# Optimization experiments

Measured on AMD Instinct MI355X. Metric: run time of the kernel, lower is better.

## Reference

```python
import jax, jax.numpy as jnp
import numpy as np
from jax import lax

DN = ('NHWC', 'HWIO', 'NHWC')
OUTPUT_STRIDE = 2
PEAK_THRESHOLD = 0.2


def setup_inputs() -> dict:
    key = jax.random.key(0)
    k1, k2, k3 = jax.random.split(key, 3)
    crops = jax.random.normal(k1, (128, 192, 192, 1), dtype=jnp.float32)
    # simple confmap backbone: stride-2 conv -> relu -> 3x3 conv to 17 nodes
    W1 = jax.random.normal(k2, (3, 3, 1, 32), dtype=jnp.float32) * 0.1
    b1 = jnp.zeros((32,), dtype=jnp.float32)
    W2 = jax.random.normal(k3, (3, 3, 32, 17), dtype=jnp.float32) * 0.1
    b2 = jnp.zeros((17,), dtype=jnp.float32)
    return {"crops": crops, "W1": W1, "b1": b1, "W2": W2, "b2": b2}


def _confmaps(crops, W1, b1, W2, b2):
    # keras_model forward: (B, 192, 192, 1) -> (B, 96, 96, 17), output_stride = 2
    h = lax.conv_general_dilated(crops, W1, (2, 2), 'SAME', dimension_numbers=DN) + b1
    h = jax.nn.relu(h)
    cms = lax.conv_general_dilated(h, W2, (1, 1), 'SAME', dimension_numbers=DN) + b2
    return cms


def _find_global_peaks_local(cms, threshold):
    # cms: (B, H, W, N) -> peaks (B, N, 2) in (x, y), vals (B, N)
    B, H, W, N = cms.shape
    cm = jnp.transpose(cms, (0, 3, 1, 2)).reshape(B, N, H * W)  # (B, N, HW)
    flat_idx = jnp.argmax(cm, axis=-1)                           # (B, N)
    vals = jnp.take_along_axis(cm, flat_idx[..., None], axis=-1)[..., 0]
    yi = flat_idx // W
    xi = flat_idx % W

    def gather(yy, xx):
        yy = jnp.clip(yy, 0, H - 1)
        xx = jnp.clip(xx, 0, W - 1)
        return jnp.take_along_axis(cm, (yy * W + xx)[..., None], axis=-1)[..., 0]

    # quarter-pixel local gradient offset (refinement='local')
    dx = 0.25 * jnp.sign(gather(yi, xi + 1) - gather(yi, xi - 1))
    dy = 0.25 * jnp.sign(gather(yi + 1, xi) - gather(yi - 1, xi))

    pts = jnp.stack([xi.astype(cm.dtype) + dx, yi.astype(cm.dtype) + dy], axis=-1)
    pts = jnp.where(vals[..., None] >= threshold, pts, jnp.nan)
    return pts, vals


def reference(crops, W1, b1, W2, b2):
    # preprocess: inputs already float grayscale, input_scale=1.0 -> identity
    cms = _confmaps(crops, W1, b1, W2, b2)
    peak_points, peak_vals = _find_global_peaks_local(cms, PEAK_THRESHOLD)
    peak_points = peak_points * OUTPUT_STRIDE  # adjust to input image grid
    # pack (x, y, val) into one array: (B, nodes, 3)
    return jnp.concatenate([peak_points, peak_vals[..., None]], axis=-1)
```

## Files before the change

kernel.cpp:

```cpp
#include <hip/hip_runtime.h>


#define NCH 17
#define C1 32
#define TW 24
#define TH 32
#define HT_W 26
#define HT_H 34
#define HSTR 28
#define IN_W 53
#define IN_H 69
#define CG 2
#define NG 16
#define NHPX (HT_H * HT_W)

typedef float v2f __attribute__((ext_vector_type(2)));

__device__ __forceinline__ unsigned long long pack_key(float v, unsigned flat) {
    unsigned ub = __float_as_uint(v);
    ub = (ub & 0x80000000u) ? ~ub : (ub | 0x80000000u);
    return ((unsigned long long)ub << 32) | (unsigned)(~flat);
}

__global__ __launch_bounds__(256, 6) void conv_peaks_kernel(
    const float* __restrict__ crops, const float* __restrict__ W1g,
    const float* __restrict__ b1g, const float* __restrict__ W2g,
    const float* __restrict__ b2g, unsigned long long* __restrict__ peaks) {
    __shared__ float s_in[IN_H * IN_W];
    __shared__ __align__(16) float s_h[CG * HT_H * HSTR];

    const int t = threadIdx.x;
    const int b = blockIdx.y;
    const int ty0 = (blockIdx.x >> 2) * TH;
    const int tx0 = (blockIdx.x & 3) * TW;
    const int iy0 = 2 * ty0 - 2;
    const int ix0 = 2 * tx0 - 2;
    const float* cb = crops + b * 192 * 192;

    for (int p = t; p < IN_H * IN_W; p += 256) {
        int r = p / IN_W, cc = p - r * IN_W;
        int iy = iy0 + r, ix = ix0 + cc;
        float v = 0.f;
        if (iy >= 0 && ix >= 0 && iy < 192 && ix < 192) v = cb[iy * 192 + ix];
        s_in[p] = v;
    }

    int in_off[4], out_off[4];
    float vf[4];
#pragma unroll
    for (int i = 0; i < 4; ++i) {
        int p = t + i * 256;
        int r = p / HT_W, cc = p - r * HT_W;
        int hy = ty0 - 1 + r, hx = tx0 - 1 + cc;
        bool valid = (hy >= 0) && (hy < 96) && (hx >= 0) && (hx < 96);
        vf[i] = valid ? 1.f : 0.f;
        in_off[i] = 2 * r * IN_W + 2 * cc;
        out_off[i] = r * HSTR + cc;
    }

    const int ly = t >> 3;
    const int lx0 = (t & 7) * 3;
    v2f acc2[8][3];
    float acc1[3];
#pragma unroll
    for (int m = 0; m < 8; ++m)
#pragma unroll
        for (int p = 0; p < 3; ++p) acc2[m][p] = (v2f)(0.f);
#pragma unroll
    for (int p = 0; p < 3; ++p) acc1[p] = 0.f;

#pragma unroll 1
    for (int g = 0; g < NG; ++g) {
        __syncthreads();

        {
            const float b10 = b1g[2 * g], b11 = b1g[2 * g + 1];
            float w10[9], w11[9];
#pragma unroll
            for (int q = 0; q < 9; ++q) {
                w10[q] = W1g[q * C1 + 2 * g];
                w11[q] = W1g[q * C1 + 2 * g + 1];
            }
#pragma unroll
            for (int i = 0; i < 4; ++i) {
                if (i < 3 || t < NHPX - 768) {
                    const float* ip = s_in + in_off[i];
                    float in9[9];
#pragma unroll
                    for (int qy = 0; qy < 3; ++qy)
#pragma unroll
                        for (int qx = 0; qx < 3; ++qx)
                            in9[qy * 3 + qx] = ip[qy * IN_W + qx];
                    float a0 = b10, a1 = b11;
#pragma unroll
                    for (int q = 0; q < 9; ++q) {
                        a0 = fmaf(in9[q], w10[q], a0);
                        a1 = fmaf(in9[q], w11[q], a1);
                    }
                    a0 = fmaxf(a0, 0.f) * vf[i];
                    a1 = fmaxf(a1, 0.f) * vf[i];
                    s_h[out_off[i]] = a0;
                    s_h[HT_H * HSTR + out_off[i]] = a1;
                }
            }
        }
        __syncthreads();

#pragma unroll
        for (int cl = 0; cl < CG; ++cl) {
            const int c = g * CG + cl;
            const float* hp = s_h + cl * (HT_H * HSTR) + ly * HSTR + lx0;
#pragma unroll
            for (int ky = 0; ky < 3; ++ky) {
                float hr[5];
#pragma unroll
                for (int j = 0; j < 5; ++j) hr[j] = hp[ky * HSTR + j];
                v2f hb[5];
#pragma unroll
                for (int j = 0; j < 5; ++j) hb[j] = (v2f){hr[j], hr[j]};
#pragma unroll
                for (int kx = 0; kx < 3; ++kx) {
                    const int k = ky * 3 + kx;
                    const float* wb = W2g + (k * C1 + c) * NCH;
                    float w[NCH];
#pragma unroll
                    for (int n = 0; n < NCH; ++n) w[n] = wb[n];
#pragma unroll
                    for (int p = 0; p < 3; ++p) {
#pragma unroll
                        for (int m = 0; m < 8; ++m) {
                            v2f wp = (v2f){w[2 * m], w[2 * m + 1]};
                            asm("v_pk_fma_f32 %0, %1, %2, %0"
                                : "+v"(acc2[m][p])
                                : "v"(hb[kx + p]), "s"(wp));
                        }
                        acc1[p] = fmaf(hr[kx + p], w[16], acc1[p]);
                    }
                }
            }
        }
    }

    const int yg = ty0 + ly, xg = tx0 + lx0;
    const int lane = t & 63;
#pragma unroll
    for (int n = 0; n < NCH; ++n) {
        const float bb = b2g[n];
        float v_[3];
#pragma unroll
        for (int p = 0; p < 3; ++p)
            v_[p] = ((n < 16) ? acc2[n >> 1][p][n & 1] : acc1[p]) + bb;
        unsigned long long pk = pack_key(v_[0], (unsigned)(yg * 96 + xg));
#pragma unroll
        for (int p = 1; p < 3; ++p) {
            unsigned long long o = pack_key(v_[p], (unsigned)(yg * 96 + xg + p));
            if (o > pk) pk = o;
        }
#pragma unroll
        for (int off = 32; off; off >>= 1) {
            unsigned long long o = __shfl_down(pk, off, 64);
            if (o > pk) pk = o;
        }
        if (lane == 0) atomicMax(&peaks[b * NCH + n], pk);
    }
}

__global__ __launch_bounds__(64) void refine_kernel(
    const float* __restrict__ crops, const float* __restrict__ W1g,
    const float* __restrict__ b1g, const float* __restrict__ W2g,
    const unsigned long long* __restrict__ peaks, float* __restrict__ out) {
    const int bn = blockIdx.x;
    const int b = bn / NCH, n = bn % NCH;
    const int lane = threadIdx.x;

    unsigned long long pk = peaks[bn];
    unsigned key = (unsigned)(pk >> 32);
    unsigned fbits = (key & 0x80000000u) ? (key ^ 0x80000000u) : ~key;
    float val = __uint_as_float(fbits);
    int flat = (int)(~(unsigned)(pk & 0xffffffffu));
    int yi = flat / 96, xi = flat - yi * 96;

    const int j = lane >> 4;
    int yy = yi + ((j == 2) ? 1 : 0) - ((j == 3) ? 1 : 0);
    int xx = xi + ((j == 0) ? 1 : 0) - ((j == 1) ? 1 : 0);
    yy = min(max(yy, 0), 95);
    xx = min(max(xx, 0), 95);

    const float* cb = crops + b * 192 * 192;
    float pat[7][7];
#pragma unroll
    for (int r = 0; r < 7; ++r) {
        int iy = 2 * yy - 2 + r;
#pragma unroll
        for (int s = 0; s < 7; ++s) {
            int ix = 2 * xx - 2 + s;
            pat[r][s] = (iy >= 0 && iy < 192 && ix >= 0 && ix < 192)
                            ? cb[iy * 192 + ix] : 0.f;
        }
    }

    float part = 0.f;
#pragma unroll
    for (int ci = 0; ci < 2; ++ci) {
        const int c = (lane & 15) + ci * 16;
        const float bias = b1g[c];
        float w1[9];
#pragma unroll
        for (int q = 0; q < 9; ++q) w1[q] = W1g[q * C1 + c];
#pragma unroll
        for (int dy = 0; dy < 3; ++dy) {
#pragma unroll
            for (int dx = 0; dx < 3; ++dx) {
                int hy = yy - 1 + dy, hx = xx - 1 + dx;
                if (hy >= 0 && hy < 96 && hx >= 0 && hx < 96) {
                    float a = bias;
#pragma unroll
                    for (int qy = 0; qy < 3; ++qy)
#pragma unroll
                        for (int qx = 0; qx < 3; ++qx)
                            a = fmaf(pat[2 * dy + qy][2 * dx + qx],
                                     w1[qy * 3 + qx], a);
                    float hval = fmaxf(a, 0.f);
                    part = fmaf(hval, W2g[((dy * 3 + dx) * C1 + c) * NCH + n], part);
                }
            }
        }
    }
    for (int off = 8; off; off >>= 1) part += __shfl_down(part, off, 16);
    float g0 = __shfl(part, 0, 64);
    float g1 = __shfl(part, 16, 64);
    float g2 = __shfl(part, 32, 64);
    float g3 = __shfl(part, 48, 64);

    if (lane == 0) {
        float d0 = g0 - g1, d1 = g2 - g3;
        float sx = (d0 > 0.f) ? 1.f : ((d0 < 0.f) ? -1.f : 0.f);
        float sy = (d1 > 0.f) ? 1.f : ((d1 < 0.f) ? -1.f : 0.f);
        float px = ((float)xi + 0.25f * sx) * 2.f;
        float py = ((float)yi + 0.25f * sy) * 2.f;
        if (!(val >= 0.2f)) {
            px = __int_as_float(0x7fc00000);
            py = __int_as_float(0x7fc00000);
        }
        out[bn * 3 + 0] = px;
        out[bn * 3 + 1] = py;
        out[bn * 3 + 2] = val;
    }
}

extern "C" void kernel_launch(void* const* d_in, const int* in_sizes, int n_in,
                              void* d_out, int out_size, void* d_ws, size_t ws_size,
                              hipStream_t stream) {
    const float* crops = (const float*)d_in[0];
    const float* W1 = (const float*)d_in[1];
    const float* b1 = (const float*)d_in[2];
    const float* W2 = (const float*)d_in[3];
    const float* b2 = (const float*)d_in[4];
    float* out = (float*)d_out;
    unsigned long long* peaks = (unsigned long long*)d_ws;

    hipMemsetAsync(d_ws, 0, 128 * NCH * sizeof(unsigned long long), stream);

    dim3 gridB(12, 128);
    conv_peaks_kernel<<<gridB, 256, 0, stream>>>(crops, W1, b1, W2, b2, peaks);
    refine_kernel<<<128 * NCH, 64, 0, stream>>>(crops, W1, b1, W2, peaks, out);
}
```

Measured before the change: 218.8 us.

## Software-pipeline conv1 channel-pair compute with conv2 accumulation, drop packed FMA

```diff
diff --git a/kernel.cpp b/kernel.cpp
--- a/kernel.cpp
+++ b/kernel.cpp
@@ -10,11 +10,8 @@
 #define HSTR 28
 #define IN_W 53
 #define IN_H 69
-#define CG 2
 #define NG 16
 #define NHPX (HT_H * HT_W)
-
-typedef float v2f __attribute__((ext_vector_type(2)));
 
 __device__ __forceinline__ unsigned long long pack_key(float v, unsigned flat) {
     unsigned ub = __float_as_uint(v);
@@ -22,12 +19,48 @@
     return ((unsigned long long)ub << 32) | (unsigned)(~flat);
 }
 
+__device__ __forceinline__ void conv1_group(
+    const float* __restrict__ W1g, const float* __restrict__ b1g,
+    const float* s_in, float* s_h, int g, int t, int ty0, int tx0) {
+    const int c0 = 2 * g, c1 = 2 * g + 1;
+    const float b10 = b1g[c0], b11 = b1g[c1];
+    float w10[9], w11[9];
+#pragma unroll
+    for (int q = 0; q < 9; ++q) {
+        w10[q] = W1g[q * C1 + c0];
+        w11[q] = W1g[q * C1 + c1];
+    }
+#pragma unroll
+    for (int i = 0; i < 4; ++i) {
+        int p = t + i * 256;
+        if (i < 3 || p < NHPX) {
+            int r = p / HT_W, cc = p - r * HT_W;
+            int hy = ty0 - 1 + r, hx = tx0 - 1 + cc;
+            float vf = (hy >= 0 && hy < 96 && hx >= 0 && hx < 96) ? 1.f : 0.f;
+            const float* ip = s_in + 2 * r * IN_W + 2 * cc;
+            float a0 = b10, a1 = b11;
+#pragma unroll
+            for (int qy = 0; qy < 3; ++qy)
+#pragma unroll
+                for (int qx = 0; qx < 3; ++qx) {
+                    float x = ip[qy * IN_W + qx];
+                    a0 = fmaf(x, w10[qy * 3 + qx], a0);
+                    a1 = fmaf(x, w11[qy * 3 + qx], a1);
+                }
+            a0 = fmaxf(a0, 0.f) * vf;
+            a1 = fmaxf(a1, 0.f) * vf;
+            s_h[r * HSTR + cc] = a0;
+            s_h[HT_H * HSTR + r * HSTR + cc] = a1;
+        }
+    }
+}
+
 __global__ __launch_bounds__(256, 6) void conv_peaks_kernel(
     const float* __restrict__ crops, const float* __restrict__ W1g,
     const float* __restrict__ b1g, const float* __restrict__ W2g,
     const float* __restrict__ b2g, unsigned long long* __restrict__ peaks) {
-    __shared__ float s_in[IN_H * IN_W];
-    __shared__ __align__(16) float s_h[CG * HT_H * HSTR];
+    __shared__ __align__(16) float s_in[IN_H * IN_W];
+    __shared__ __align__(16) float s_h[2 * HT_H * HSTR];
 
     const int t = threadIdx.x;
     const int b = blockIdx.y;
@@ -44,98 +77,73 @@
         if (iy >= 0 && ix >= 0 && iy < 192 && ix < 192) v = cb[iy * 192 + ix];
         s_in[p] = v;
     }
-
-    int in_off[4], out_off[4];
-    float vf[4];
-#pragma unroll
-    for (int i = 0; i < 4; ++i) {
-        int p = t + i * 256;
-        int r = p / HT_W, cc = p - r * HT_W;
-        int hy = ty0 - 1 + r, hx = tx0 - 1 + cc;
-        bool valid = (hy >= 0) && (hy < 96) && (hx >= 0) && (hx < 96);
-        vf[i] = valid ? 1.f : 0.f;
-        in_off[i] = 2 * r * IN_W + 2 * cc;
-        out_off[i] = r * HSTR + cc;
-    }
+    __syncthreads();
+    conv1_group(W1g, b1g, s_in, s_h, 0, t, ty0, tx0);
 
     const int ly = t >> 3;
     const int lx0 = (t & 7) * 3;
-    v2f acc2[8][3];
-    float acc1[3];
-#pragma unroll
-    for (int m = 0; m < 8; ++m)
-#pragma unroll
-        for (int p = 0; p < 3; ++p) acc2[m][p] = (v2f)(0.f);
-#pragma unroll
-    for (int p = 0; p < 3; ++p) acc1[p] = 0.f;
+    const float* hpbase = s_h + ly * HSTR + lx0;
+    float acc[NCH][3];
+#pragma unroll
+    for (int n = 0; n < NCH; ++n)
+#pragma unroll
+        for (int p = 0; p < 3; ++p) acc[n][p] = 0.f;
 
 #pragma unroll 1
     for (int g = 0; g < NG; ++g) {
         __syncthreads();
 
         {
-            const float b10 = b1g[2 * g], b11 = b1g[2 * g + 1];
-            float w10[9], w11[9];
-#pragma unroll
-            for (int q = 0; q < 9; ++q) {
-                w10[q] = W1g[q * C1 + 2 * g];
-                w11[q] = W1g[q * C1 + 2 * g + 1];
+            float hr[3][5];
+#pragma unroll
+            for (int ky = 0; ky < 3; ++ky)
+#pragma unroll
+                for (int j = 0; j < 5; ++j) hr[ky][j] = hpbase[ky * HSTR + j];
+            const int c = 2 * g;
+#pragma unroll
+            for (int k = 0; k < 9; ++k) {
+                const int ky = k / 3, kx = k - ky * 3;
+                const float* wb = W2g + (k * C1 + c) * NCH;
+                float w[NCH];
+#pragma unroll
+                for (int n = 0; n < NCH; ++n) w[n] = wb[n];
+#pragma unroll
+                for (int p = 0; p < 3; ++p) {
+                    const float h = hr[ky][kx + p];
+#pragma unroll
+                    for (int n = 0; n < NCH; ++n)
+                        acc[n][p] = fmaf(h, w[n], acc[n][p]);
+                }
             }
-#pragma unroll
-            for (int i = 0; i < 4; ++i) {
-                if (i < 3 || t < NHPX - 768) {
-                    const float* ip = s_in + in_off[i];
-                    float in9[9];
-#pragma unroll
-                    for (int qy = 0; qy < 3; ++qy)
-#pragma unroll
-                        for (int qx = 0; qx < 3; ++qx)
-                            in9[qy * 3 + qx] = ip[qy * IN_W + qx];
-                    float a0 = b10, a1 = b11;
-#pragma unroll
-                    for (int q = 0; q < 9; ++q) {
-                        a0 = fmaf(in9[q], w10[q], a0);
-                        a1 = fmaf(in9[q], w11[q], a1);
-                    }
-                    a0 = fmaxf(a0, 0.f) * vf[i];
-                    a1 = fmaxf(a1, 0.f) * vf[i];
-                    s_h[out_off[i]] = a0;
-                    s_h[HT_H * HSTR + out_off[i]] = a1;
-                }
-            }
-        }
+        }
+
+        float hr1[3][5];
+#pragma unroll
+        for (int ky = 0; ky < 3; ++ky)
+#pragma unroll
+            for (int j = 0; j < 5; ++j)
+                hr1[ky][j] = hpbase[HT_H * HSTR + ky * HSTR + j];
+
         __syncthreads();
 
-#pragma unroll
-        for (int cl = 0; cl < CG; ++cl) {
-            const int c = g * CG + cl;
-            const float* hp = s_h + cl * (HT_H * HSTR) + ly * HSTR + lx0;
-#pragma unroll
-            for (int ky = 0; ky < 3; ++ky) {
-                float hr[5];
-#pragma unroll
-                for (int j = 0; j < 5; ++j) hr[j] = hp[ky * HSTR + j];
-                v2f hb[5];
-#pragma unroll
-                for (int j = 0; j < 5; ++j) hb[j] = (v2f){hr[j], hr[j]};
-#pragma unroll
-                for (int kx = 0; kx < 3; ++kx) {
-                    const int k = ky * 3 + kx;
-                    const float* wb = W2g + (k * C1 + c) * NCH;
-                    float w[NCH];
-#pragma unroll
-                    for (int n = 0; n < NCH; ++n) w[n] = wb[n];
-#pragma unroll
-                    for (int p = 0; p < 3; ++p) {
-#pragma unroll
-                        for (int m = 0; m < 8; ++m) {
-                            v2f wp = (v2f){w[2 * m], w[2 * m + 1]};
-                            asm("v_pk_fma_f32 %0, %1, %2, %0"
-                                : "+v"(acc2[m][p])
-                                : "v"(hb[kx + p]), "s"(wp));
-                        }
-                        acc1[p] = fmaf(hr[kx + p], w[16], acc1[p]);
-                    }
+        if (g < NG - 1)
+            conv1_group(W1g, b1g, s_in, s_h, g + 1, t, ty0, tx0);
+
+        {
+            const int c = 2 * g + 1;
+#pragma unroll
+            for (int k = 0; k < 9; ++k) {
+                const int ky = k / 3, kx = k - ky * 3;
+                const float* wb = W2g + (k * C1 + c) * NCH;
+                float w[NCH];
+#pragma unroll
+                for (int n = 0; n < NCH; ++n) w[n] = wb[n];
+#pragma unroll
+                for (int p = 0; p < 3; ++p) {
+                    const float h = hr1[ky][kx + p];
+#pragma unroll
+                    for (int n = 0; n < NCH; ++n)
+                        acc[n][p] = fmaf(h, w[n], acc[n][p]);
                 }
             }
         }
@@ -146,14 +154,10 @@
 #pragma unroll
     for (int n = 0; n < NCH; ++n) {
         const float bb = b2g[n];
-        float v_[3];
-#pragma unroll
-        for (int p = 0; p < 3; ++p)
-            v_[p] = ((n < 16) ? acc2[n >> 1][p][n & 1] : acc1[p]) + bb;
-        unsigned long long pk = pack_key(v_[0], (unsigned)(yg * 96 + xg));
+        unsigned long long pk = pack_key(acc[n][0] + bb, (unsigned)(yg * 96 + xg));
 #pragma unroll
         for (int p = 1; p < 3; ++p) {
-            unsigned long long o = pack_key(v_[p], (unsigned)(yg * 96 + xg + p));
+            unsigned long long o = pack_key(acc[n][p] + bb, (unsigned)(yg * 96 + xg + p));
             if (o > pk) pk = o;
         }
 #pragma unroll
```

Measured after the change: 280.7 us. +28.3%, slower.
